# Kernel optimization log

Hardware: AMD Instinct MI355X
Metric: run time of the kernel (lower is better)

## Reference

```python
import jax, jax.numpy as jnp
import numpy as np

H = 1024          # hidden_size
I = 2048          # intermediate_size
E = 8             # num_experts
K = 2             # num_experts_per_token
B, S = 4, 4096


def setup_inputs() -> dict:
    key = jax.random.key(0)
    ks = jax.random.split(key, 5)
    scale = 0.02
    return {
        "hidden_states": jax.random.normal(ks[0], (B, S, H), dtype=jnp.float32),
        "gate_w": jax.random.normal(ks[1], (H, E), dtype=jnp.float32) * scale,      # router gate (Linear, no bias), stored [in,out]
        "gate_proj_w": jax.random.normal(ks[2], (E, H, I), dtype=jnp.float32) * scale,
        "up_proj_w": jax.random.normal(ks[3], (E, H, I), dtype=jnp.float32) * scale,
        "down_proj_w": jax.random.normal(ks[4], (E, I, H), dtype=jnp.float32) * scale,
    }


def reference(hidden_states, gate_w, gate_proj_w, up_proj_w, down_proj_w):
    b, s, h = hidden_states.shape
    x = hidden_states.reshape(-1, h)                      # (T, H), T = b*s
    T = x.shape[0]

    # --- Router: softmax over experts, top-k, renormalize ---
    logits = x @ gate_w                                    # (T, E)
    probs = jax.nn.softmax(logits, axis=-1)
    topk_w, topk_idx = jax.lax.top_k(probs, K)             # (T, K)
    topk_w = topk_w / jnp.sum(topk_w, axis=-1, keepdims=True)

    # Per-token combine weight for each expert (0 if not routed).
    # topk indices are distinct, so scatter-add == scatter-set here.
    combine = jnp.zeros((T, E), dtype=x.dtype).at[
        jnp.arange(T)[:, None], topk_idx
    ].add(topk_w)                                          # (T, E)

    # --- Experts: SwiGLU FFN, weighted combine ---
    out = jnp.zeros_like(x)
    for e in range(E):  # small fixed expert count
        g = jax.nn.silu(x @ gate_proj_w[e])                # (T, I)
        u = x @ up_proj_w[e]                               # (T, I)
        y = (g * u) @ down_proj_w[e]                       # (T, H)
        out = out + y * combine[:, e:e + 1]
    return out.reshape(b, s, h)
```

## Files before the change

kernel.cpp:

```cpp
#include <hip/hip_runtime.h>
#include <hip/hip_bf16.h>

#define T_TOK 16384
#define H_DIM 1024
#define I_DIM 2048
#define E_NUM 8

typedef short short8 __attribute__((ext_vector_type(8)));
typedef float f32x4 __attribute__((ext_vector_type(4)));

__device__ __forceinline__ unsigned short f2bf(float f) {
  union { float f; unsigned u; } v; v.f = f;
  unsigned r = (v.u + 0x7FFFu + ((v.u >> 16) & 1u)) >> 16;
  return (unsigned short)r;
}
__device__ __forceinline__ float bf2f(unsigned short u) {
  union { unsigned u; float f; } v; v.u = ((unsigned)u) << 16;
  return v.f;
}

__device__ __forceinline__ void gload16(const void* g, void* l) {
  __builtin_amdgcn_global_load_lds(
      (const __attribute__((address_space(1))) unsigned int*)g,
      (__attribute__((address_space(3))) unsigned int*)l, 16, 0, 0);
}

#define VMCNT4() asm volatile("s_waitcnt vmcnt(4)" ::: "memory")
#define VMCNT0() asm volatile("s_waitcnt vmcnt(0)" ::: "memory")
#define LGKM0()  asm volatile("s_waitcnt lgkmcnt(0)" ::: "memory")
#define BAR() __builtin_amdgcn_s_barrier()
#define SCHEDFENCE() __builtin_amdgcn_sched_barrier(0)
#define PRIO1() __builtin_amdgcn_s_setprio(1)
#define PRIO0() __builtin_amdgcn_s_setprio(0)

__global__ __launch_bounds__(256) void convert_router_kernel(
    const float* __restrict__ x, const float* __restrict__ gw,
    unsigned short* __restrict__ xb,
    int* __restrict__ tke, float* __restrict__ pwv) {
  const int tid = threadIdx.x;
  const int lane = tid & 63;
  const int wv = tid >> 6;
  const int t = blockIdx.x * 4 + wv;
  const float* xr = x + (size_t)t * H_DIM;
  unsigned short* xbr = xb + (size_t)t * H_DIM;

  float acc[8] = {0.f, 0.f, 0.f, 0.f, 0.f, 0.f, 0.f, 0.f};
#pragma unroll
  for (int i = 0; i < 4; ++i) {
    int h0 = i * 256 + lane * 4;
    float4 v = *(const float4*)(xr + h0);
    ushort4 o;
    o.x = f2bf(v.x); o.y = f2bf(v.y); o.z = f2bf(v.z); o.w = f2bf(v.w);
    *(ushort4*)(xbr + h0) = o;
    float vv[4] = {v.x, v.y, v.z, v.w};
#pragma unroll
    for (int j = 0; j < 4; ++j) {
      const float4 g0 = *(const float4*)(gw + (size_t)(h0 + j) * 8);
      const float4 g1 = *(const float4*)(gw + (size_t)(h0 + j) * 8 + 4);
      acc[0] += vv[j] * g0.x; acc[1] += vv[j] * g0.y;
      acc[2] += vv[j] * g0.z; acc[3] += vv[j] * g0.w;
      acc[4] += vv[j] * g1.x; acc[5] += vv[j] * g1.y;
      acc[6] += vv[j] * g1.z; acc[7] += vv[j] * g1.w;
    }
  }
#pragma unroll
  for (int e = 0; e < 8; ++e) {
#pragma unroll
    for (int off = 32; off; off >>= 1) acc[e] += __shfl_xor(acc[e], off);
  }
  int e1 = 0; float l1 = acc[0];
#pragma unroll
  for (int e = 1; e < 8; ++e) if (acc[e] > l1) { l1 = acc[e]; e1 = e; }
  int first_non = (e1 == 0) ? 1 : 0;
  int e2 = first_non; float l2 = acc[first_non];
#pragma unroll
  for (int e = 0; e < 8; ++e) {
    if (e == e1 || e == first_non) continue;
    if (acc[e] > l2) { l2 = acc[e]; e2 = e; }
  }
  float r = expf(l2 - l1);
  float w1 = 1.f / (1.f + r);
  float w2 = r / (1.f + r);
  if (lane == 0) {
    pwv[2 * t] = w1;
    pwv[2 * t + 1] = w2;
    tke[t] = e1 | (e2 << 4);
  }
}

__global__ __launch_bounds__(256) void build_lists_kernel(
    const int* __restrict__ tke, int* __restrict__ list, int* __restrict__ cnt) {
  const int t = blockIdx.x * 256 + threadIdx.x;
  const int lane = threadIdx.x & 63;
  const int pk = tke[t];
  const int ee[2] = {pk & 15, (pk >> 4) & 15};
#pragma unroll
  for (int phase = 0; phase < 2; ++phase) {
    const int e = ee[phase];
    const int pid = 2 * t + phase;
#pragma unroll
    for (int ex = 0; ex < E_NUM; ++ex) {
      unsigned long long mask = __ballot(e == ex);
      if (e == ex) {
        unsigned long long below = mask & ((1ull << lane) - 1ull);
        int rank = __popcll(below);
        int leader = __ffsll((unsigned long long)mask) - 1;
        int base = 0;
        if (lane == leader) base = atomicAdd(&cnt[ex], __popcll(mask));
        base = __shfl(base, leader);
        list[ex * T_TOK + base + rank] = pid;
      }
    }
  }
}

__global__ __launch_bounds__(256) void transpose_convert(
    const float* __restrict__ src, unsigned short* __restrict__ dst, int K, int N) {
  __shared__ float t[128][65];
  const int e = blockIdx.x, kt = blockIdx.y, nt = blockIdx.z;
  const float* s = src + (size_t)e * K * N + (size_t)(kt * 128) * N + nt * 64;
  unsigned short* d = dst + (size_t)e * N * K + (size_t)(nt * 64) * K + kt * 128;
  const int tid = threadIdx.x;
  const int lr = tid & 15, row = tid >> 4;
#pragma unroll
  for (int p = 0; p < 8; ++p) {
    int k = row + p * 16;
    float4 v = *(const float4*)(s + (size_t)k * N + lr * 4);
    t[k][lr * 4 + 0] = v.x;
    t[k][lr * 4 + 1] = v.y;
    t[k][lr * 4 + 2] = v.z;
    t[k][lr * 4 + 3] = v.w;
  }
  __syncthreads();
  const int kc = tid & 15, nr = tid >> 4;
#pragma unroll
  for (int p = 0; p < 4; ++p) {
    int n = nr + p * 16;
    short8 o;
#pragma unroll
    for (int j = 0; j < 8; ++j) o[j] = (short)f2bf(t[kc * 8 + j][n]);
    *(short8*)&d[(size_t)n * K + kc * 8] = o;
  }
}

__global__ __launch_bounds__(256, 3) void gemm_gateup(
    const unsigned short* __restrict__ xb, const unsigned short* __restrict__ wgt,
    const unsigned short* __restrict__ wut, const int* __restrict__ list,
    const int* __restrict__ cnt, const float* __restrict__ pwv,
    unsigned short* __restrict__ hbuf) {
  __shared__ unsigned short As[2][128 * 32];
  __shared__ unsigned short Bg[2][64 * 32];
  __shared__ unsigned short Bu[2][64 * 32];
  __shared__ int rows_s[128];
  __shared__ float pws[128];

  const int tid = threadIdx.x;
  const int e = blockIdx.y >> 7;
  const int mt = blockIdx.y & 127;
  const int ce = cnt[e];
  if (mt * 128 >= ce) return;
  const int n0 = blockIdx.x * 64;

  if (tid < 128) {
    int idx = mt * 128 + tid;
    int pid = list[e * T_TOK + (idx < ce ? idx : 0)];
    rows_s[tid] = pid;
    pws[tid] = pwv[pid];
  }
  __syncthreads();

  const int s0 = tid, s1 = 256 + tid;
  const int q0 = (((s0 & 3) ^ ((s0 >> 3) & 3)) * 8);
  const int q1 = (((s1 & 3) ^ ((s1 >> 3) & 3)) * 8);
  const int tok0 = rows_s[s0 >> 2] >> 1, tok1 = rows_s[s1 >> 2] >> 1;

  const unsigned short* wg_base = wgt + ((size_t)e * I_DIM + n0) * H_DIM;
  const unsigned short* wu_base = wut + ((size_t)e * I_DIM + n0) * H_DIM;
  const unsigned short* a_src0 = xb + (size_t)tok0 * H_DIM + q0;
  const unsigned short* a_src1 = xb + (size_t)tok1 * H_DIM + q1;
  const unsigned short* g_src0 = wg_base + (size_t)(s0 >> 2) * H_DIM + q0;
  const unsigned short* u_src0 = wu_base + (size_t)(s0 >> 2) * H_DIM + q0;

#define STAGE_GU(b, k0)                         \
  do {                                          \
    gload16(a_src0 + (k0), &As[b][s0 * 8]);     \
    gload16(a_src1 + (k0), &As[b][s1 * 8]);     \
    gload16(g_src0 + (k0), &Bg[b][s0 * 8]);     \
    gload16(u_src0 + (k0), &Bu[b][s0 * 8]);     \
  } while (0)

  f32x4 zero = {0.f, 0.f, 0.f, 0.f};
  f32x4 accg[4][2], accu[4][2];
#pragma unroll
  for (int m = 0; m < 4; ++m)
#pragma unroll
    for (int n = 0; n < 2; ++n) { accg[m][n] = zero; accu[m][n] = zero; }

  const int lane = tid & 63;
  const int wv = tid >> 6;
  const int wr = (wv >> 1) * 64;
  const int wc = (wv & 1) * 32;
  const int lr = lane & 15;
  const int lks = (((lane >> 4) ^ ((lr >> 1) & 3)) * 8);

  STAGE_GU(0, 0);

  for (int kt = 0; kt < H_DIM / 32; ++kt) {
    const int cur = kt & 1;
    if (kt < H_DIM / 32 - 1) {
      STAGE_GU(cur ^ 1, (kt + 1) * 32);
      VMCNT4();
    } else {
      VMCNT0();
    }
    BAR();
    SCHEDFENCE();
    const unsigned short* Ab = As[cur];
    const unsigned short* Bgb = Bg[cur];
    const unsigned short* Bub = Bu[cur];
    short8 a[4], bg[2], bu[2];
#pragma unroll
    for (int m = 0; m < 4; ++m)
      a[m] = *(const short8*)&Ab[(wr + m * 16 + lr) * 32 + lks];
#pragma unroll
    for (int n = 0; n < 2; ++n) {
      bg[n] = *(const short8*)&Bgb[(wc + n * 16 + lr) * 32 + lks];
      bu[n] = *(const short8*)&Bub[(wc + n * 16 + lr) * 32 + lks];
    }
    PRIO1();
#pragma unroll
    for (int m = 0; m < 4; ++m)
#pragma unroll
      for (int n = 0; n < 2; ++n) {
        accg[m][n] = __builtin_amdgcn_mfma_f32_16x16x32_bf16(a[m], bg[n], accg[m][n], 0, 0, 0);
        accu[m][n] = __builtin_amdgcn_mfma_f32_16x16x32_bf16(a[m], bu[n], accu[m][n], 0, 0, 0);
      }
    PRIO0();
    BAR();
  }
#undef STAGE_GU

  const int rr = (lane >> 4) * 4;
#pragma unroll
  for (int m = 0; m < 4; ++m) {
#pragma unroll
    for (int j = 0; j < 4; ++j) {
      int tr = wr + m * 16 + rr + j;
      if (mt * 128 + tr < ce) {
        int pid = rows_s[tr];
        float wgt_r = pws[tr];
        size_t rowb = (size_t)pid * I_DIM + n0 + wc;
#pragma unroll
        for (int n = 0; n < 2; ++n) {
          float g = accg[m][n][j];
          float u = accu[m][n][j];
          float hv = wgt_r * (g / (1.f + __expf(-g))) * u;
          hbuf[rowb + n * 16 + lr] = f2bf(hv);
        }
      }
    }
  }
}

__global__ __launch_bounds__(512, 2) void gemm_down8(
    const unsigned short* __restrict__ hbuf, const unsigned short* __restrict__ wdt,
    const int* __restrict__ list, const int* __restrict__ cnt,
    unsigned short* __restrict__ pbuf) {
  __shared__ unsigned short As[2][256 * 64];
  __shared__ unsigned short Bs[2][256 * 64];
  __shared__ int rows_s[256];

  const int tid = threadIdx.x;
  const int e = blockIdx.y >> 6;
  const int mt = blockIdx.y & 63;
  const int ce = cnt[e];
  if (mt * 256 >= ce) return;
  const int n0 = blockIdx.x * 256;

  if (tid < 256) {
    int idx = mt * 256 + tid;
    rows_s[tid] = list[e * T_TOK + (idx < ce ? idx : 0)];
  }
  __syncthreads();

  const unsigned short* wd_base = wdt + ((size_t)e * H_DIM + n0) * I_DIM;
  const unsigned short* a_base[4];
  const unsigned short* b_base[4];
#pragma unroll
  for (int j = 0; j < 4; ++j) {
    int slot = j * 512 + tid;
    int row = slot >> 3;
    int cs = ((slot & 7) ^ (row & 7)) * 8;
    a_base[j] = hbuf + (size_t)rows_s[row] * I_DIM + cs;
    b_base[j] = wd_base + (size_t)row * I_DIM + cs;
  }

#define STAGE8(b, t)                                          \
  do {                                                        \
    const int k0_ = (t) * 64;                                 \
    gload16(a_base[0] + k0_, &As[b][(0 * 512 + tid) * 8]);    \
    gload16(a_base[1] + k0_, &As[b][(1 * 512 + tid) * 8]);    \
    gload16(a_base[2] + k0_, &As[b][(2 * 512 + tid) * 8]);    \
    gload16(a_base[3] + k0_, &As[b][(3 * 512 + tid) * 8]);    \
    gload16(b_base[0] + k0_, &Bs[b][(0 * 512 + tid) * 8]);    \
    gload16(b_base[1] + k0_, &Bs[b][(1 * 512 + tid) * 8]);    \
    gload16(b_base[2] + k0_, &Bs[b][(2 * 512 + tid) * 8]);    \
    gload16(b_base[3] + k0_, &Bs[b][(3 * 512 + tid) * 8]);    \
  } while (0)

  f32x4 zero = {0.f, 0.f, 0.f, 0.f};
  f32x4 acc[8][4];
#pragma unroll
  for (int m = 0; m < 8; ++m)
#pragma unroll
    for (int n = 0; n < 4; ++n) acc[m][n] = zero;

  const int lane = tid & 63;
  const int wv = tid >> 6;
  const int wm = wv >> 2;
  const int wn = wv & 3;
  const int lr = lane & 15;
  const int lg = lane >> 4;
  const int pc0 = ((lg) ^ (lr & 7)) * 8;
  const int pc1 = ((lg + 4) ^ (lr & 7)) * 8;

  short8 a[4][2], b[4][2];

  STAGE8(0, 0);

  const int NT = I_DIM / 64;
  for (int t = 0; t < NT; ++t) {
    const int cur = t & 1;
    VMCNT0();
    BAR();
    SCHEDFENCE();
    if (t + 1 < NT) STAGE8(cur ^ 1, t + 1);

    const unsigned short* Ab = As[cur];
    const unsigned short* Bb = Bs[cur];

#pragma unroll
    for (int m = 0; m < 4; ++m) {
      int row = (wm * 128 + m * 16 + lr) * 64;
      a[m][0] = *(const short8*)&Ab[row + pc0];
      a[m][1] = *(const short8*)&Ab[row + pc1];
    }
#pragma unroll
    for (int n = 0; n < 2; ++n) {
      int row = (wn * 64 + n * 16 + lr) * 64;
      b[n][0] = *(const short8*)&Bb[row + pc0];
      b[n][1] = *(const short8*)&Bb[row + pc1];
    }
    BAR(); LGKM0();
    PRIO1();
#pragma unroll
    for (int m = 0; m < 4; ++m)
#pragma unroll
      for (int n = 0; n < 2; ++n) {
        acc[m][n] = __builtin_amdgcn_mfma_f32_16x16x32_bf16(a[m][0], b[n][0], acc[m][n], 0, 0, 0);
        acc[m][n] = __builtin_amdgcn_mfma_f32_16x16x32_bf16(a[m][1], b[n][1], acc[m][n], 0, 0, 0);
      }
    PRIO0();

#pragma unroll
    for (int n = 2; n < 4; ++n) {
      int row = (wn * 64 + n * 16 + lr) * 64;
      b[n][0] = *(const short8*)&Bb[row + pc0];
      b[n][1] = *(const short8*)&Bb[row + pc1];
    }
    BAR(); LGKM0();
    PRIO1();
#pragma unroll
    for (int m = 0; m < 4; ++m)
#pragma unroll
      for (int n = 2; n < 4; ++n) {
        acc[m][n] = __builtin_amdgcn_mfma_f32_16x16x32_bf16(a[m][0], b[n][0], acc[m][n], 0, 0, 0);
        acc[m][n] = __builtin_amdgcn_mfma_f32_16x16x32_bf16(a[m][1], b[n][1], acc[m][n], 0, 0, 0);
      }
    PRIO0();

#pragma unroll
    for (int m = 0; m < 4; ++m) {
      int row = (wm * 128 + (m + 4) * 16 + lr) * 64;
      a[m][0] = *(const short8*)&Ab[row + pc0];
      a[m][1] = *(const short8*)&Ab[row + pc1];
    }
    BAR(); LGKM0();
    PRIO1();
#pragma unroll
    for (int m = 0; m < 4; ++m)
#pragma unroll
      for (int n = 0; n < 2; ++n) {
        acc[m + 4][n] = __builtin_amdgcn_mfma_f32_16x16x32_bf16(a[m][0], b[n][0], acc[m + 4][n], 0, 0, 0);
        acc[m + 4][n] = __builtin_amdgcn_mfma_f32_16x16x32_bf16(a[m][1], b[n][1], acc[m + 4][n], 0, 0, 0);
      }
    PRIO0();

    PRIO1();
#pragma unroll
    for (int m = 0; m < 4; ++m)
#pragma unroll
      for (int n = 2; n < 4; ++n) {
        acc[m + 4][n] = __builtin_amdgcn_mfma_f32_16x16x32_bf16(a[m][0], b[n][0], acc[m + 4][n], 0, 0, 0);
        acc[m + 4][n] = __builtin_amdgcn_mfma_f32_16x16x32_bf16(a[m][1], b[n][1], acc[m + 4][n], 0, 0, 0);
      }
    PRIO0();
  }
#undef STAGE8

  const int rr = lg * 4;
#pragma unroll
  for (int m = 0; m < 8; ++m) {
#pragma unroll
    for (int j = 0; j < 4; ++j) {
      int tr = wm * 128 + m * 16 + rr + j;
      if (mt * 256 + tr < ce) {
        int pid = rows_s[tr];
        unsigned short* orow = pbuf + (size_t)pid * H_DIM + n0 + wn * 64;
#pragma unroll
        for (int n = 0; n < 4; ++n)
          orow[n * 16 + lr] = f2bf(acc[m][n][j]);
      }
    }
  }
}

__global__ __launch_bounds__(256) void combine_kernel(float* __restrict__ out) {
  const int tid = threadIdx.x, lane = tid & 63, wv = tid >> 6;
  const int t = blockIdx.x * 4 + wv;
  const unsigned short* p = (const unsigned short*)out;
  const unsigned short* r0 = p + (size_t)(2 * t) * H_DIM + lane * 16;
  const unsigned short* r1 = p + (size_t)(2 * t + 1) * H_DIM + lane * 16;
  short8 a0 = *(const short8*)r0;
  short8 a1 = *(const short8*)(r0 + 8);
  short8 b0 = *(const short8*)r1;
  short8 b1 = *(const short8*)(r1 + 8);
  float res[16];
#pragma unroll
  for (int j = 0; j < 8; ++j) {
    res[j] = bf2f((unsigned short)a0[j]) + bf2f((unsigned short)b0[j]);
    res[8 + j] = bf2f((unsigned short)a1[j]) + bf2f((unsigned short)b1[j]);
  }
  float* orow = out + (size_t)t * H_DIM + lane * 16;
#pragma unroll
  for (int j = 0; j < 4; ++j) {
    float4 w = {res[4 * j], res[4 * j + 1], res[4 * j + 2], res[4 * j + 3]};
    ((float4*)orow)[j] = w;
  }
}

extern "C" void kernel_launch(void* const* d_in, const int* in_sizes, int n_in,
                              void* d_out, int out_size, void* d_ws, size_t ws_size,
                              hipStream_t stream) {
  const float* x = (const float*)d_in[0];
  const float* gw = (const float*)d_in[1];
  const float* wgf = (const float*)d_in[2];
  const float* wuf = (const float*)d_in[3];
  const float* wdf = (const float*)d_in[4];

  const size_t off_xb   = 0;
  const size_t off_wdt  = 33554432;
  const size_t off_h    = 67108864;
  const size_t off_list = 201326592;
  const size_t off_pw   = 201850880;
  const size_t off_cnt  = 201981952;
  const size_t ws_needed = off_cnt + 64;
  if (ws_size < ws_needed) return;

  char* ws = (char*)d_ws;
  unsigned short* xb   = (unsigned short*)(ws + off_xb);
  unsigned short* wdt  = (unsigned short*)(ws + off_wdt);
  unsigned short* hbuf = (unsigned short*)(ws + off_h);
  int*   list = (int*)(ws + off_list);
  float* pwv  = (float*)(ws + off_pw);
  int*   cnt  = (int*)(ws + off_cnt);
  int*   tke  = (int*)(ws + off_h);

  unsigned short* wgt = (unsigned short*)d_out;
  unsigned short* wut = (unsigned short*)d_out + (size_t)E_NUM * H_DIM * I_DIM;
  unsigned short* pbuf = (unsigned short*)d_out;

  hipMemsetAsync(cnt, 0, E_NUM * sizeof(int), stream);

  convert_router_kernel<<<T_TOK / 4, 256, 0, stream>>>(x, gw, xb, tke, pwv);
  build_lists_kernel<<<T_TOK / 256, 256, 0, stream>>>(tke, list, cnt);
  transpose_convert<<<dim3(E_NUM, H_DIM / 128, I_DIM / 64), 256, 0, stream>>>(
      wgf, wgt, H_DIM, I_DIM);
  transpose_convert<<<dim3(E_NUM, H_DIM / 128, I_DIM / 64), 256, 0, stream>>>(
      wuf, wut, H_DIM, I_DIM);
  transpose_convert<<<dim3(E_NUM, I_DIM / 128, H_DIM / 64), 256, 0, stream>>>(
      wdf, wdt, I_DIM, H_DIM);

  gemm_gateup<<<dim3(I_DIM / 64, E_NUM * 128), 256, 0, stream>>>(
      xb, wgt, wut, list, cnt, pwv, hbuf);

  gemm_down8<<<dim3(H_DIM / 256, E_NUM * 64), 512, 0, stream>>>(
      hbuf, wdt, list, cnt, pbuf);

  combine_kernel<<<T_TOK / 4, 256, 0, stream>>>((float*)d_out);
}
```

Baseline: 760.2 us.

## Interleave down-GEMM global loads with MFMA phases and swizzle block mapping

The down-projection kernel now spreads next-tile global-to-LDS loads across its MFMA sub-phases with partial vmcnt waits and extra barriers, and remaps the block index so tiles are swizzled across expert/row tiles. The gate/up kernel drops its early prefetch with vmcnt(4) and instead waits for all loads, then issues the next stage after the barrier, removing the trailing barrier. The router kernel switches from float4 loads to per-lane scalar loads of x. These are several unrelated changes aimed at overlapping memory with compute and improving cache locality, at the cost of more barriers and possibly less latency hiding in the gate/up kernel.

Result: faster. 723.3 us (-4.9%).

```diff
diff --git a/kernel.cpp b/kernel.cpp
--- a/kernel.cpp
+++ b/kernel.cpp
@@ -26,6 +26,7 @@
 }
 
 #define VMCNT4() asm volatile("s_waitcnt vmcnt(4)" ::: "memory")
+#define VMCNT2() asm volatile("s_waitcnt vmcnt(2)" ::: "memory")
 #define VMCNT0() asm volatile("s_waitcnt vmcnt(0)" ::: "memory")
 #define LGKM0()  asm volatile("s_waitcnt lgkmcnt(0)" ::: "memory")
 #define BAR() __builtin_amdgcn_s_barrier()
@@ -46,22 +47,16 @@
 
   float acc[8] = {0.f, 0.f, 0.f, 0.f, 0.f, 0.f, 0.f, 0.f};
 #pragma unroll
-  for (int i = 0; i < 4; ++i) {
-    int h0 = i * 256 + lane * 4;
-    float4 v = *(const float4*)(xr + h0);
-    ushort4 o;
-    o.x = f2bf(v.x); o.y = f2bf(v.y); o.z = f2bf(v.z); o.w = f2bf(v.w);
-    *(ushort4*)(xbr + h0) = o;
-    float vv[4] = {v.x, v.y, v.z, v.w};
-#pragma unroll
-    for (int j = 0; j < 4; ++j) {
-      const float4 g0 = *(const float4*)(gw + (size_t)(h0 + j) * 8);
-      const float4 g1 = *(const float4*)(gw + (size_t)(h0 + j) * 8 + 4);
-      acc[0] += vv[j] * g0.x; acc[1] += vv[j] * g0.y;
-      acc[2] += vv[j] * g0.z; acc[3] += vv[j] * g0.w;
-      acc[4] += vv[j] * g1.x; acc[5] += vv[j] * g1.y;
-      acc[6] += vv[j] * g1.z; acc[7] += vv[j] * g1.w;
-    }
+  for (int i = 0; i < 16; ++i) {
+    const int h = i * 64 + lane;
+    float xv = xr[h];
+    xbr[h] = f2bf(xv);
+    const float4 g0 = *(const float4*)(gw + (size_t)h * 8);
+    const float4 g1 = *(const float4*)(gw + (size_t)h * 8 + 4);
+    acc[0] += xv * g0.x; acc[1] += xv * g0.y;
+    acc[2] += xv * g0.z; acc[3] += xv * g0.w;
+    acc[4] += xv * g1.x; acc[5] += xv * g1.y;
+    acc[6] += xv * g1.z; acc[7] += xv * g1.w;
   }
 #pragma unroll
   for (int e = 0; e < 8; ++e) {
@@ -207,14 +202,10 @@
 
   for (int kt = 0; kt < H_DIM / 32; ++kt) {
     const int cur = kt & 1;
-    if (kt < H_DIM / 32 - 1) {
-      STAGE_GU(cur ^ 1, (kt + 1) * 32);
-      VMCNT4();
-    } else {
-      VMCNT0();
-    }
+    VMCNT0();
     BAR();
     SCHEDFENCE();
+    if (kt < H_DIM / 32 - 1) STAGE_GU(cur ^ 1, (kt + 1) * 32);
     const unsigned short* Ab = As[cur];
     const unsigned short* Bgb = Bg[cur];
     const unsigned short* Bub = Bu[cur];
@@ -236,7 +227,6 @@
         accu[m][n] = __builtin_amdgcn_mfma_f32_16x16x32_bf16(a[m], bu[n], accu[m][n], 0, 0, 0);
       }
     PRIO0();
-    BAR();
   }
 #undef STAGE_GU
 
@@ -271,11 +261,15 @@
   __shared__ int rows_s[256];
 
   const int tid = threadIdx.x;
-  const int e = blockIdx.y >> 6;
-  const int mt = blockIdx.y & 63;
+  const int flat = blockIdx.x + 4 * blockIdx.y;
+  const int sw = (flat & 7) * (2048 / 8) + (flat >> 3);
+  const int ntile = sw & 3;
+  const int mb = sw >> 2;
+  const int e = mb >> 6;
+  const int mt = mb & 63;
   const int ce = cnt[e];
   if (mt * 256 >= ce) return;
-  const int n0 = blockIdx.x * 256;
+  const int n0 = ntile * 256;
 
   if (tid < 256) {
     int idx = mt * 256 + tid;
@@ -295,17 +289,15 @@
     b_base[j] = wd_base + (size_t)row * I_DIM + cs;
   }
 
-#define STAGE8(b, t)                                          \
-  do {                                                        \
-    const int k0_ = (t) * 64;                                 \
-    gload16(a_base[0] + k0_, &As[b][(0 * 512 + tid) * 8]);    \
-    gload16(a_base[1] + k0_, &As[b][(1 * 512 + tid) * 8]);    \
-    gload16(a_base[2] + k0_, &As[b][(2 * 512 + tid) * 8]);    \
-    gload16(a_base[3] + k0_, &As[b][(3 * 512 + tid) * 8]);    \
-    gload16(b_base[0] + k0_, &Bs[b][(0 * 512 + tid) * 8]);    \
-    gload16(b_base[1] + k0_, &Bs[b][(1 * 512 + tid) * 8]);    \
-    gload16(b_base[2] + k0_, &Bs[b][(2 * 512 + tid) * 8]);    \
-    gload16(b_base[3] + k0_, &Bs[b][(3 * 512 + tid) * 8]);    \
+#define LD_A(b, t, j0, j1)                                     \
+  do {                                                         \
+    gload16(a_base[j0] + (t) * 64, &As[b][(j0 * 512 + tid) * 8]); \
+    gload16(a_base[j1] + (t) * 64, &As[b][(j1 * 512 + tid) * 8]); \
+  } while (0)
+#define LD_B(b, t, j0, j1)                                     \
+  do {                                                         \
+    gload16(b_base[j0] + (t) * 64, &Bs[b][(j0 * 512 + tid) * 8]); \
+    gload16(b_base[j1] + (t) * 64, &Bs[b][(j1 * 512 + tid) * 8]); \
   } while (0)
 
   f32x4 zero = {0.f, 0.f, 0.f, 0.f};
@@ -326,15 +318,17 @@
 
   short8 a[4][2], b[4][2];
 
-  STAGE8(0, 0);
+  LD_A(0, 0, 0, 1); LD_A(0, 0, 2, 3);
+  LD_B(0, 0, 0, 1); LD_B(0, 0, 2, 3);
 
   const int NT = I_DIM / 64;
   for (int t = 0; t < NT; ++t) {
     const int cur = t & 1;
-    VMCNT0();
+    const int nxt = cur ^ 1;
+    const bool more = (t + 1 < NT);
+    if (more) { LD_A(nxt, t + 1, 0, 1); VMCNT2(); } else { VMCNT0(); }
     BAR();
     SCHEDFENCE();
-    if (t + 1 < NT) STAGE8(cur ^ 1, t + 1);
 
     const unsigned short* Ab = As[cur];
     const unsigned short* Bb = Bs[cur];
@@ -351,7 +345,9 @@
       b[n][0] = *(const short8*)&Bb[row + pc0];
       b[n][1] = *(const short8*)&Bb[row + pc1];
     }
+    if (more) LD_A(nxt, t + 1, 2, 3);
     BAR(); LGKM0();
+    SCHEDFENCE();
     PRIO1();
 #pragma unroll
     for (int m = 0; m < 4; ++m)
@@ -361,6 +357,7 @@
         acc[m][n] = __builtin_amdgcn_mfma_f32_16x16x32_bf16(a[m][1], b[n][1], acc[m][n], 0, 0, 0);
       }
     PRIO0();
+    BAR();
 
 #pragma unroll
     for (int n = 2; n < 4; ++n) {
@@ -368,7 +365,9 @@
       b[n][0] = *(const short8*)&Bb[row + pc0];
       b[n][1] = *(const short8*)&Bb[row + pc1];
     }
+    if (more) LD_B(nxt, t + 1, 0, 1);
     BAR(); LGKM0();
+    SCHEDFENCE();
     PRIO1();
 #pragma unroll
     for (int m = 0; m < 4; ++m)
@@ -378,6 +377,7 @@
         acc[m][n] = __builtin_amdgcn_mfma_f32_16x16x32_bf16(a[m][1], b[n][1], acc[m][n], 0, 0, 0);
       }
     PRIO0();
+    BAR();
 
 #pragma unroll
     for (int m = 0; m < 4; ++m) {
@@ -385,7 +385,9 @@
       a[m][0] = *(const short8*)&Ab[row + pc0];
       a[m][1] = *(const short8*)&Ab[row + pc1];
     }
+    if (more) LD_B(nxt, t + 1, 2, 3);
     BAR(); LGKM0();
+    SCHEDFENCE();
     PRIO1();
 #pragma unroll
     for (int m = 0; m < 4; ++m)
@@ -395,6 +397,7 @@
         acc[m + 4][n] = __builtin_amdgcn_mfma_f32_16x16x32_bf16(a[m][1], b[n][1], acc[m + 4][n], 0, 0, 0);
       }
     PRIO0();
+    BAR();
 
     PRIO1();
 #pragma unroll
@@ -405,8 +408,10 @@
         acc[m + 4][n] = __builtin_amdgcn_mfma_f32_16x16x32_bf16(a[m][1], b[n][1], acc[m + 4][n], 0, 0, 0);
       }
     PRIO0();
-  }
-#undef STAGE8
+    BAR();
+  }
+#undef LD_A
+#undef LD_B
 
   const int rr = lg * 4;
 #pragma unroll
```
